# Optimization experiments

Measured on AMD Instinct MI355X. Metric: run time of the kernel, lower is better.

The kernel has to match this reference:

```python
import jax, jax.numpy as jnp
import numpy as np

N_USER = 805   # herbs
N_ITEM = 390   # symptoms
N = 1195       # total nodes
D = 64         # embedding_dim (forced by final matmul)
E = 1_000_000
E_SUB = 500_000
B = 2048
BN_EPS = 1e-5


def _gcn(x, W, b, edge):
    # GCNConv_SH: message = Linear(x_j), aggr='mean', then tanh.
    # Linear commutes with mean (bias included when in-degree>0; isolated nodes -> 0),
    # so transform nodes once, then gather->segment-mean.
    h = x @ W.T + b                      # [N, D]
    src, dst = edge[0], edge[1]
    agg = jax.ops.segment_sum(h[src], dst, num_segments=N)          # [N, D]
    cnt = jax.ops.segment_sum(jnp.ones(edge.shape[1], x.dtype), dst, num_segments=N)
    mean = agg / jnp.maximum(cnt, 1.0)[:, None]   # isolated nodes stay 0 (PyG mean aggr)
    return jnp.tanh(mean)


def _two_layer(x, W1, b1, W2, b2, edge):
    return _gcn(_gcn(x, W1, b1, edge), W2, b2, edge)


def _norm(x, axis):
    # self.Norm(emb, count, n_dim): L2 normalize along n_dim (0 for user side, 1 for item side)
    return x / jnp.linalg.norm(x, axis=axis, keepdims=True)


def setup_inputs() -> dict:
    key = jax.random.key(0)
    ks = jax.random.split(key, 12)
    emb = jax.random.normal(ks[0], (N, D), jnp.float32)
    s = 1.0 / np.sqrt(D)
    W1 = jax.random.normal(ks[1], (D, D), jnp.float32) * s
    b1 = jnp.zeros((D,), jnp.float32)
    W2 = jax.random.normal(ks[2], (D, D), jnp.float32) * s
    b2 = jnp.zeros((D,), jnp.float32)
    mlp_W = jax.random.normal(ks[3], (64, D), jnp.float32) * s
    mlp_b = jnp.zeros((64,), jnp.float32)
    bn_gamma = jnp.ones((64,), jnp.float32)
    bn_beta = jnp.zeros((64,), jnp.float32)
    # multi-hot prescription; guarantee nonzero row sums for the mean-pool divide
    presc = (jax.random.uniform(ks[4], (B, N_ITEM)) < 0.05).astype(jnp.float32)
    presc = presc.at[:, 0].set(1.0)
    total_g = jax.random.randint(ks[5], (2, E), 0, N)
    sub_g1 = jax.random.randint(ks[6], (2, E_SUB), 0, N)
    sub_g2 = jax.random.randint(ks[7], (2, E_SUB), 0, N)
    edge_index_SH = jax.random.randint(ks[8], (2, 1000), 0, N)
    return {"edge_index_SH": edge_index_SH, "prescription": presc,
            "emb": emb, "W1": W1, "b1": b1, "W2": W2, "b2": b2,
            "mlp_W": mlp_W, "mlp_b": mlp_b, "bn_gamma": bn_gamma, "bn_beta": bn_beta,
            "total_g": total_g, "sub_g1": sub_g1, "sub_g2": sub_g2}


def reference(edge_index_SH, prescription, emb, W1, b1, W2, b2, mlp_W, mlp_b,
              bn_gamma, bn_beta, total_g, sub_g1, sub_g2):
    # edge_index_SH is accepted (forward signature) but unused, as in the source.
    x_SH1 = emb                                   # SH_embedding(arange(1195))
    x_SH6 = _two_layer(emb, W1, b1, W2, b2, total_g)   # two shared GCNConv_SH layers
    SH_g3 = _two_layer(emb, W1, b1, W2, b2, sub_g1)
    SH_g33 = _two_layer(emb, W1, b1, W2, b2, sub_g2)

    # ssl_layer_loss returns normalized previous (raw-embedding) views
    s_u = _norm(x_SH1[:N_USER], 0)   # [805, D]
    s_i = _norm(x_SH1[N_USER:], 1)   # [390, D]
    # sgl_loss returns normalized sub-graph-1 views
    n_u = _norm(SH_g3[:N_USER], 0)
    n_i = _norm(SH_g3[N_USER:], 1)
    # Same2Loss (reconstructed): fuse all contrastive views into final node reps
    c_u = 0.25 * (s_i + n_i + _norm(x_SH6[N_USER:], 1) + _norm(SH_g33[N_USER:], 1))  # [390, D]
    c_i = 0.25 * (s_u + n_u + _norm(x_SH6[:N_USER], 0) + _norm(SH_g33[:N_USER], 0))  # [805, D]

    e_synd = prescription @ c_u                           # [B, D]
    e_synd = e_synd / prescription.sum(axis=1, keepdims=True)
    h = e_synd @ mlp_W.T + mlp_b                          # [B, 64]
    mu = h.mean(axis=0)
    var = h.var(axis=0)                                   # biased, as torch BN training
    h = (h - mu) / jnp.sqrt(var + BN_EPS) * bn_gamma + bn_beta
    h = jax.nn.relu(h)
    pre = h @ c_i.T                                       # [B, 805]
    return pre
```

## Files before the change

### kernel.cpp

```cpp
#include <hip/hip_runtime.h>
#include <hip/hip_bf16.h>


#define NN    1195
#define NUSER 805
#define NITEM 390
#define DD    64
#define BB    2048
#define NPAD  1216
#define E_TOT 1000000
#define E_SUB 500000
#define MT    19
#define KT    8
#define CHUNK 3
#define LSTR  72
#define OUT2STRIDE (NN*DD)
#define CPG    299
#define P8W    152
#define ROWS   96
#define RB     13
#define FNT    13
#define KPAD   448
#define ENT    7

typedef unsigned int uint;
typedef unsigned short u16;
typedef unsigned char u8;
typedef __attribute__((ext_vector_type(8))) short short8;
typedef __attribute__((ext_vector_type(4))) float f32x4;

__device__ __forceinline__ float wsum(float v) {
#pragma unroll
    for (int m = 32; m > 0; m >>= 1) v += __shfl_xor(v, m, 64);
    return v;
}
__device__ __forceinline__ u16 f2b(float f) {
    uint u = __float_as_uint(f);
    return (u16)((u + 0x7FFFu + ((u >> 16) & 1u)) >> 16);
}
__device__ __forceinline__ float b2f16(u16 b) { return __uint_as_float(((uint)b) << 16); }
__device__ __forceinline__ void split4(const float* v, u16* hh, u16* ll) {
#pragma unroll
    for (int j = 0; j < 4; ++j) {
        u16 h = f2b(v[j]);
        hh[j] = h;
        ll[j] = f2b(v[j] - b2f16(h));
    }
}
__device__ __forceinline__ uint2 pack4(const u16* x) {
    uint2 o;
    o.x = (uint)x[0] | ((uint)x[1] << 16);
    o.y = (uint)x[2] | ((uint)x[3] << 16);
    return o;
}

#define CVT_EMB   0
#define CVT_W1    76480
#define CVT_B1    80576
#define CVT_W2    80640
#define CVT_B2    84736
#define CVT_MLPW  84800
#define CVT_MLPB  88896
#define CVT_GAMMA 88960
#define CVT_BETA  89024
#define CVT_TOTAL 89088

constexpr size_t alignUp64(size_t x) { return (x + 63) & ~size_t(63); }
constexpr size_t OFF_BNS  = 0;
constexpr size_t OFF_CNSS = 128;
constexpr size_t OFF_FLAG = 384;
constexpr size_t OFF_CVT  = 448;
constexpr size_t OFF_ABF  = alignUp64(OFF_CVT + CVT_TOTAL);
constexpr size_t OFF_RC   = alignUp64(OFF_ABF + (3ull * NN * NPAD) / 2);
constexpr size_t OFF_POOL = alignUp64(OFF_RC + 3ull * NPAD);
constexpr size_t OFF_PART = OFF_POOL;
constexpr size_t OFF_H1   = alignUp64(OFF_PART + (size_t)KT * 3 * NPAD * 64);
constexpr size_t OFF_H2   = alignUp64(OFF_H1 + 64ull * NPAD);
constexpr size_t OFF_OUT2 = alignUp64(OFF_H2 + 3ull * 64 * NPAD);
constexpr size_t OFF_CU   = alignUp64(OFF_OUT2 + 3ull * NN * DD);
constexpr size_t OFF_CI   = alignUp64(OFF_CU + 448ull * DD);
constexpr size_t OFF_H    = alignUp64(OFF_CI + (size_t)NUSER * DD);
constexpr size_t POOL_END = alignUp64(OFF_H + (size_t)BB * DD);


__global__ __launch_bounds__(512) void k_front(const void* presc, const void* emb,
        const void* p1, const void* p2, const void* p3, const void* p4,
        const void* p5, const void* p6, const void* p7, const void* p8, const void* p9,
        const int* __restrict__ tg, const int* __restrict__ s1, const int* __restrict__ s2,
        float* __restrict__ dst, float* __restrict__ cnss, float* __restrict__ bnsum,
        int* __restrict__ flag, uint* __restrict__ P8, int S, int HB) {
    __shared__ __align__(16) uint lds[ROWS * P8W];
    int b = blockIdx.x, t = threadIdx.x;
    int isbf = (((const u16*)presc)[0] == 0x3F80u) ? 1 : 0;
    if (b < HB) {
        int p = b % S;
        int rg = b / S;
        int r = rg % RB;
        int g = rg / RB;
        int r0 = r * ROWS;
        {
            uint4* l4 = (uint4*)lds;
            for (int i = t; i < (ROWS * P8W) >> 2; i += 512) l4[i] = (uint4){0u, 0u, 0u, 0u};
        }
        __syncthreads();
        const int* eg = (g == 0) ? tg : (g == 1 ? s1 : s2);
        int Eg = (g == 0) ? E_TOT : E_SUB;
        int e0 = (int)(((long)p * Eg / S) & ~3L);
        int e1 = (p == S - 1) ? Eg : (int)(((long)(p + 1) * Eg / S) & ~3L);
        const int* srcp = eg;
        const int* dstp = eg + Eg;
        for (int i = e0 + t * 4; i < e1; i += 512 * 4) {
            int4 d4 = *(const int4*)(dstp + i);
            int4 s4 = *(const int4*)(srcp + i);
            int rw;
            rw = d4.x - r0; if ((unsigned)rw < ROWS) atomicAdd(&lds[rw * P8W + (s4.x >> 3)], 1u << ((s4.x & 7) * 4));
            rw = d4.y - r0; if ((unsigned)rw < ROWS) atomicAdd(&lds[rw * P8W + (s4.y >> 3)], 1u << ((s4.y & 7) * 4));
            rw = d4.z - r0; if ((unsigned)rw < ROWS) atomicAdd(&lds[rw * P8W + (s4.z >> 3)], 1u << ((s4.z & 7) * 4));
            rw = d4.w - r0; if ((unsigned)rw < ROWS) atomicAdd(&lds[rw * P8W + (s4.w >> 3)], 1u << ((s4.w & 7) * 4));
        }
        __syncthreads();
        int rmax = ROWS; if (r0 + rmax > NN) rmax = NN - r0;
        uint* out = P8 + ((size_t)p * 3 + g) * NN * P8W + (size_t)r0 * P8W;
        int n4 = (rmax * P8W) >> 2;
        const uint4* l4 = (const uint4*)lds;
        uint4* o4 = (uint4*)out;
        for (int i = t; i < n4; i += 512) o4[i] = l4[i];
    } else if (b == HB) {
        for (int i = t; i < 192; i += 512) cnss[64 + i] = 0.0f;
        if (t < 128) bnsum[t] = 0.0f;
        int c = t & 63, chunk = t >> 6;
        float s = 0.0f;
        const u16* e16 = (const u16*)emb;
        const float* e32 = (const float*)emb;
        for (int r = chunk; r < NUSER; r += 8) {
            float v = isbf ? b2f16(e16[r * 64 + c]) : e32[r * 64 + c];
            s = fmaf(v, v, s);
        }
        float* sd = (float*)lds;
        sd[t] = s;
        __syncthreads();
        if (t < 64) {
            float tot = 0.0f;
#pragma unroll
            for (int j = 0; j < 8; ++j) tot += sd[j * 64 + t];
            cnss[t] = tot;
        }
    } else {
        int i = (b - HB - 1) * 512 + t;
        if (i == 0) *flag = isbf;
        if (i < CVT_TOTAL) {
            const void* s2p; int o2;
            if      (i < CVT_W1)    { s2p = p1; o2 = i; }
            else if (i < CVT_B1)    { s2p = p2; o2 = i - CVT_W1; }
            else if (i < CVT_W2)    { s2p = p3; o2 = i - CVT_B1; }
            else if (i < CVT_B2)    { s2p = p4; o2 = i - CVT_W2; }
            else if (i < CVT_MLPW)  { s2p = p5; o2 = i - CVT_B2; }
            else if (i < CVT_MLPB)  { s2p = p6; o2 = i - CVT_MLPW; }
            else if (i < CVT_GAMMA) { s2p = p7; o2 = i - CVT_MLPB; }
            else if (i < CVT_BETA)  { s2p = p8; o2 = i - CVT_GAMMA; }
            else                    { s2p = p9; o2 = i - CVT_BETA; }
            dst[i] = isbf ? __bfloat162float(((const __hip_bfloat16*)s2p)[o2])
                          : ((const float*)s2p)[o2];
        }
    }
}

__device__ __forceinline__ void xf2_body(int g, int n0, int t,
        const float* xsrc, size_t xgstride,
        const float* part, const float* rcnt, int fromPart, int rowlim,
        const float* W, const float* bias,
        u16* Hhi, u16* Hlo, size_t hgstride, int ostride,
        u16* Ah, u16* Al, u16* Bh, u16* Bl, float* bs) {
    int w = t >> 6, l = t & 63;
    if (t < 64) bs[t] = bias ? bias[t] : 0.0f;
    int r = t >> 2, c0 = (t & 3) * 16;
    {
        const float* Wr = W + r * 64 + c0;
        float av[16];
#pragma unroll
        for (int j4 = 0; j4 < 4; ++j4) {
            float4 v = *(const float4*)(Wr + j4 * 4);
            av[j4*4+0] = v.x; av[j4*4+1] = v.y; av[j4*4+2] = v.z; av[j4*4+3] = v.w;
        }
#pragma unroll
        for (int j4 = 0; j4 < 4; ++j4) {
            u16 hh[4], ll[4];
            split4(av + j4*4, hh, ll);
            *(uint2*)(Ah + r * LSTR + c0 + j4*4) = pack4(hh);
            *(uint2*)(Al + r * LSTR + c0 + j4*4) = pack4(ll);
        }
    }
    {
        int node = n0 + r;
        float xr[16];
#pragma unroll
        for (int j = 0; j < 16; ++j) xr[j] = 0.0f;
        if (node < rowlim) {
            if (fromPart) {
#pragma unroll
                for (int k = 0; k < KT; ++k) {
                    const float* pp = part + (((size_t)k * 3 + g) * NPAD + node) * 64 + c0;
#pragma unroll
                    for (int j4 = 0; j4 < 4; ++j4) {
                        float4 v = *(const float4*)(pp + j4 * 4);
                        xr[j4*4+0] += v.x; xr[j4*4+1] += v.y;
                        xr[j4*4+2] += v.z; xr[j4*4+3] += v.w;
                    }
                }
                float rc = rcnt[g * NPAD + node];
#pragma unroll
                for (int j = 0; j < 16; ++j) xr[j] = tanhf(xr[j] * rc);
            } else {
                const float* Xr = xsrc + xgstride * g + (size_t)node * 64 + c0;
#pragma unroll
                for (int j4 = 0; j4 < 4; ++j4) {
                    float4 v = *(const float4*)(Xr + j4 * 4);
                    xr[j4*4+0] = v.x; xr[j4*4+1] = v.y;
                    xr[j4*4+2] = v.z; xr[j4*4+3] = v.w;
                }
            }
        }
#pragma unroll
        for (int j4 = 0; j4 < 4; ++j4) {
            u16 hh[4], ll[4];
            split4(xr + j4*4, hh, ll);
            *(uint2*)(Bh + r * LSTR + c0 + j4*4) = pack4(hh);
            *(uint2*)(Bl + r * LSTR + c0 + j4*4) = pack4(ll);
        }
    }
    __syncthreads();
    f32x4 acc[4];
#pragma unroll
    for (int p = 0; p < 4; ++p) acc[p] = (f32x4){0.f, 0.f, 0.f, 0.f};
    int mrow = w * 16 + (l & 15);
    int q8 = (l >> 4) * 8;
#pragma unroll
    for (int ks = 0; ks < 2; ++ks) {
        short8 ah = *(const short8*)(Ah + mrow * LSTR + ks * 32 + q8);
        short8 al = *(const short8*)(Al + mrow * LSTR + ks * 32 + q8);
#pragma unroll
        for (int p = 0; p < 4; ++p) {
            int nrow = p * 16 + (l & 15);
            short8 bh = *(const short8*)(Bh + nrow * LSTR + ks * 32 + q8);
            short8 bl = *(const short8*)(Bl + nrow * LSTR + ks * 32 + q8);
            acc[p] = __builtin_amdgcn_mfma_f32_16x16x32_bf16(ah, bh, acc[p], 0, 0, 0);
            acc[p] = __builtin_amdgcn_mfma_f32_16x16x32_bf16(ah, bl, acc[p], 0, 0, 0);
            acc[p] = __builtin_amdgcn_mfma_f32_16x16x32_bf16(al, bh, acc[p], 0, 0, 0);
        }
    }
    int q = l >> 4;
#pragma unroll
    for (int p = 0; p < 4; ++p) {
        int node = n0 + p * 16 + (l & 15);
#pragma unroll
        for (int rr2 = 0; rr2 < 4; ++rr2) {
            int d = w * 16 + q * 4 + rr2;
            float v = acc[p][rr2] + bs[d];
            u16 h = f2b(v);
            size_t o = hgstride * g + (size_t)d * ostride + node;
            Hhi[o] = h;
            Hlo[o] = f2b(v - b2f16(h));
        }
    }
}

__global__ __launch_bounds__(256) void k_xf2(const float* __restrict__ xsrc,
        size_t xgstride, const float* __restrict__ part, const float* __restrict__ rcnt,
        int fromPart, int ngb, int rowlim,
        const float* __restrict__ W, const float* __restrict__ bias,
        u16* __restrict__ Hhi, u16* __restrict__ Hlo, size_t hgstride, int ostride) {
    __shared__ u16 Ah[64 * LSTR], Al[64 * LSTR], Bh[64 * LSTR], Bl[64 * LSTR];
    __shared__ float bs[64];
    int b = blockIdx.x;
    xf2_body(b / ngb, (b % ngb) * 64, threadIdx.x, xsrc, xgstride, part, rcnt,
             fromPart, rowlim, W, bias, Hhi, Hlo, hgstride, ostride,
             Ah, Al, Bh, Bl, bs);
}

__global__ __launch_bounds__(256) void k_abf_xf1(const uint* __restrict__ P8, int S,
        u16* __restrict__ Abf, float* __restrict__ rcnt,
        const float* __restrict__ embF, const float* __restrict__ W1,
        const float* __restrict__ b1, u16* __restrict__ H1hi, u16* __restrict__ H1lo) {
    __shared__ u16 Ah[64 * LSTR], Al[64 * LSTR], Bh[64 * LSTR], Bl[64 * LSTR];
    __shared__ float bs[64];
    __shared__ float ws4[4];
    int b = blockIdx.x, t = threadIdx.x;
    if (b < 3 * NN) {
        int g = b / NN, m = b % NN;
        int w = t >> 6;
        float partial = 0.0f;
        if (t < P8W) {
            uint cnt[8] = {0, 0, 0, 0, 0, 0, 0, 0};
            for (int p = 0; p < S; ++p) {
                uint v = P8[(((size_t)p * 3 + g) * NN + m) * P8W + t];
#pragma unroll
                for (int k = 0; k < 8; ++k) cnt[k] += (v >> (4 * k)) & 15u;
            }
            uint4 o;
            o.x = (uint)f2b((float)cnt[0]) | ((uint)f2b((float)cnt[1]) << 16);
            o.y = (uint)f2b((float)cnt[2]) | ((uint)f2b((float)cnt[3]) << 16);
            o.z = (uint)f2b((float)cnt[4]) | ((uint)f2b((float)cnt[5]) << 16);
            o.w = (uint)f2b((float)cnt[6]) | ((uint)f2b((float)cnt[7]) << 16);
            *(uint4*)(Abf + (size_t)b * NPAD + t * 8) = o;
#pragma unroll
            for (int k = 0; k < 8; ++k) partial += (float)cnt[k];
        }
        partial = wsum(partial);
        if ((t & 63) == 0) ws4[w] = partial;
        __syncthreads();
        if (t == 0)
            rcnt[g * NPAD + m] = 1.0f / fmaxf(ws4[0] + ws4[1] + ws4[2] + ws4[3], 1.0f);
    } else {
        int nt = b - 3 * NN;
        xf2_body(0, nt * 64, t, embF, 0, nullptr, nullptr, 0, NN, W1, b1,
                 H1hi, H1lo, 0, NPAD, Ah, Al, Bh, Bl, bs);
    }
}

__global__ __launch_bounds__(256) void k_aggp(const u16* __restrict__ Abf,
        const u16* __restrict__ Hhi, const u16* __restrict__ Hlo, size_t hstride,
        float* __restrict__ part) {
    int b = blockIdx.x;
    int kt = b & 7;
    int mt = (b >> 3) % MT;
    int g  = (b >> 3) / MT;
    int t = threadIdx.x, w = t >> 6, l = t & 63;
    __shared__ u16 As[64 * LSTR], Bh[64 * LSTR], Bl[64 * LSTR];
    f32x4 acc[4];
#pragma unroll
    for (int p = 0; p < 4; ++p) acc[p] = (f32x4){0.f, 0.f, 0.f, 0.f};
    int m0 = mt * 64;
    const u16* Ag = Abf + (size_t)g * NN * NPAD;
    const u16* Hg = Hhi + hstride * g;
    const u16* Lg = Hlo + hstride * g;
    int st0 = kt * CHUNK;
    int st1 = st0 + CHUNK; if (st1 > MT) st1 = MT;
    int rr = t >> 4, c4 = (t & 15) * 4;
    for (int st = st0; st < st1; ++st) {
        int s0 = st * 64;
        __syncthreads();
#pragma unroll
        for (int pass = 0; pass < 4; ++pass) {
            int r = pass * 16 + rr;
            uint2 av = {0u, 0u};
            if (m0 + r < NN) av = *(const uint2*)(Ag + (size_t)(m0 + r) * NPAD + s0 + c4);
            *(uint2*)(As + r * LSTR + c4) = av;
            *(uint2*)(Bh + r * LSTR + c4) = *(const uint2*)(Hg + (size_t)r * NPAD + s0 + c4);
            *(uint2*)(Bl + r * LSTR + c4) = *(const uint2*)(Lg + (size_t)r * NPAD + s0 + c4);
        }
        __syncthreads();
        int mrow = w * 16 + (l & 15);
        int q8 = (l >> 4) * 8;
#pragma unroll
        for (int ks = 0; ks < 2; ++ks) {
            short8 a = *(const short8*)(As + mrow * LSTR + ks * 32 + q8);
#pragma unroll
            for (int p = 0; p < 4; ++p) {
                int nrow = p * 16 + (l & 15);
                short8 bh = *(const short8*)(Bh + nrow * LSTR + ks * 32 + q8);
                short8 bl = *(const short8*)(Bl + nrow * LSTR + ks * 32 + q8);
                acc[p] = __builtin_amdgcn_mfma_f32_16x16x32_bf16(a, bh, acc[p], 0, 0, 0);
                acc[p] = __builtin_amdgcn_mfma_f32_16x16x32_bf16(a, bl, acc[p], 0, 0, 0);
            }
        }
    }
    int q = l >> 4;
#pragma unroll
    for (int p = 0; p < 4; ++p) {
        int n = p * 16 + (l & 15);
#pragma unroll
        for (int r = 0; r < 4; ++r) {
            int m = m0 + w * 16 + q * 4 + r;
            if (m < NN)
                part[(((size_t)kt * 3 + g) * NPAD + m) * 64 + n] = acc[p][r];
        }
    }
}

__global__ __launch_bounds__(256) void k_comb(const float* __restrict__ part,
        const float* __restrict__ rcnt, float* __restrict__ out, float* __restrict__ cnss) {
    int g = blockIdx.x / CPG, bi = blockIdx.x % CPG;
    int t = threadIdx.x;
    int idx = bi * 256 + t;
    int m = idx >> 6, n = idx & 63;
    bool valid = idx < NN * 64;
    float v = 0.0f;
    if (valid) {
        float s = 0.0f;
#pragma unroll
        for (int k = 0; k < KT; ++k)
            s += part[(((size_t)k * 3 + g) * NPAD + m) * 64 + n];
        v = tanhf(s * rcnt[g * NPAD + m]);
        out[(size_t)g * NN * 64 + idx] = v;
    }
    float x2 = (valid && m < NUSER) ? v * v : 0.0f;
    __shared__ float sd[256];
    sd[t] = x2;
    __syncthreads();
    if (t < 64) {
        float s = sd[t] + sd[t + 64] + sd[t + 128] + sd[t + 192];
        if (s != 0.0f) atomicAdd(&cnss[(g + 1) * 64 + t], s);
    }
}

__global__ void k_cuci(const float* __restrict__ embf, const float* __restrict__ out2,
                       const float* __restrict__ cnss, float* __restrict__ cu,
                       float* __restrict__ ci) {
    int b = blockIdx.x, l = threadIdx.x;
    if (b < 448) {
        if (b >= NITEM) { cu[(size_t)b * DD + l] = 0.0f; return; }
        int node = NUSER + b;
        const float* v0 = embf + (size_t)node * DD;
        const float* v1 = out2 + (size_t)node * DD;
        const float* v2 = out2 + OUT2STRIDE + (size_t)node * DD;
        const float* v3 = out2 + 2ull * OUT2STRIDE + (size_t)node * DD;
        float total = 0.0f;
        { float x = v0[l]; float ss = wsum(x * x); total += x / sqrtf(ss); }
        { float x = v1[l]; float ss = wsum(x * x); total += x / sqrtf(ss); }
        { float x = v2[l]; float ss = wsum(x * x); total += x / sqrtf(ss); }
        { float x = v3[l]; float ss = wsum(x * x); total += x / sqrtf(ss); }
        cu[(size_t)b * DD + l] = 0.25f * total;
    } else {
        int u = b - 448;
        size_t i = (size_t)u * DD + l;
        float s = embf[i] / sqrtf(cnss[l])
                + out2[i] / sqrtf(cnss[64 + l])
                + out2[OUT2STRIDE + i] / sqrtf(cnss[128 + l])
                + out2[2ull * OUT2STRIDE + i] / sqrtf(cnss[192 + l]);
        ci[i] = 0.25f * s;
    }
}

__global__ __launch_bounds__(256) void k_esynd(const void* __restrict__ presc,
        const u16* __restrict__ cwh, const u16* __restrict__ cwl,
        const float* __restrict__ mlpB, const int* __restrict__ flag,
        float* __restrict__ hpre, float* __restrict__ bnsum) {
    int m0 = blockIdx.x * 64;
    int t = threadIdx.x, w = t >> 6, l = t & 63;
    int isbf = *flag;
    const u16* pB = (const u16*)presc;
    const float* pF = (const float*)presc;
    __shared__ u16 As[64 * LSTR], Bh[64 * LSTR], Bl[64 * LSTR];
    __shared__ u16 Ones[16 * LSTR];
    __shared__ float bs[64];
    __shared__ float r1[4][64], r2[4][64];
    for (int i = t; i < 16 * LSTR; i += 256) Ones[i] = (i < 64) ? 0x3F80u : 0u;
    if (t < 64) bs[t] = mlpB[t];

    f32x4 acc[4], acc1;
#pragma unroll
    for (int p = 0; p < 4; ++p) acc[p] = (f32x4){0.f, 0.f, 0.f, 0.f};
    acc1 = (f32x4){0.f, 0.f, 0.f, 0.f};

    int rr = t >> 4, c4 = (t & 15) * 4;
    for (int st = 0; st < ENT; ++st) {
        int s0 = st * 64;
        __syncthreads();
#pragma unroll
        for (int pass = 0; pass < 4; ++pass) {
            int r = pass * 16 + rr;
            int m = m0 + r;
            int kb = s0 + c4;
            u16 a4[4];
            if (kb + 3 < NITEM) {
                if (isbf) {
                    const uint* p32 = (const uint*)pB + (((size_t)m * NITEM + kb) >> 1);
                    uint u0 = p32[0], u1 = p32[1];
                    a4[0] = (u16)u0; a4[1] = (u16)(u0 >> 16);
                    a4[2] = (u16)u1; a4[3] = (u16)(u1 >> 16);
                } else {
                    const float2* pf2 = (const float2*)(pF + (size_t)m * NITEM + kb);
                    float2 f0 = pf2[0], f1 = pf2[1];
                    a4[0] = f2b(f0.x); a4[1] = f2b(f0.y);
                    a4[2] = f2b(f1.x); a4[3] = f2b(f1.y);
                }
            } else {
#pragma unroll
                for (int j = 0; j < 4; ++j) {
                    int k = kb + j;
                    a4[j] = (k < NITEM)
                          ? (isbf ? pB[(size_t)m * NITEM + k] : f2b(pF[(size_t)m * NITEM + k]))
                          : (u16)0;
                }
            }
            uint2 o;
            o.x = (uint)a4[0] | ((uint)a4[1] << 16);
            o.y = (uint)a4[2] | ((uint)a4[3] << 16);
            *(uint2*)(As + r * LSTR + c4) = o;
            *(uint2*)(Bh + r * LSTR + c4) = *(const uint2*)(cwh + (size_t)r * KPAD + s0 + c4);
            *(uint2*)(Bl + r * LSTR + c4) = *(const uint2*)(cwl + (size_t)r * KPAD + s0 + c4);
        }
        __syncthreads();
        int mrow = w * 16 + (l & 15);
        int q8 = (l >> 4) * 8;
#pragma unroll
        for (int ks = 0; ks < 2; ++ks) {
            short8 a = *(const short8*)(As + mrow * LSTR + ks * 32 + q8);
            short8 on = *(const short8*)(Ones + (l & 15) * LSTR + ks * 32 + q8);
            acc1 = __builtin_amdgcn_mfma_f32_16x16x32_bf16(a, on, acc1, 0, 0, 0);
#pragma unroll
            for (int p = 0; p < 4; ++p) {
                int nrow = p * 16 + (l & 15);
                short8 bh = *(const short8*)(Bh + nrow * LSTR + ks * 32 + q8);
                short8 bl = *(const short8*)(Bl + nrow * LSTR + ks * 32 + q8);
                acc[p] = __builtin_amdgcn_mfma_f32_16x16x32_bf16(a, bh, acc[p], 0, 0, 0);
                acc[p] = __builtin_amdgcn_mfma_f32_16x16x32_bf16(a, bl, acc[p], 0, 0, 0);
            }
        }
    }
    float inv[4];
#pragma unroll
    for (int r = 0; r < 4; ++r)
        inv[r] = 1.0f / __shfl(acc1[r], l & 48, 64);
    int q = l >> 4;
#pragma unroll
    for (int p = 0; p < 4; ++p) {
        int col = p * 16 + (l & 15);
        float a = 0.0f, c = 0.0f;
#pragma unroll
        for (int r = 0; r < 4; ++r) {
            float hv = acc[p][r] * inv[r] + bs[col];
            hpre[(size_t)(m0 + w * 16 + q * 4 + r) * DD + col] = hv;
            a += hv; c = fmaf(hv, hv, c);
        }
        a += __shfl_xor(a, 16, 64); a += __shfl_xor(a, 32, 64);
        c += __shfl_xor(c, 16, 64); c += __shfl_xor(c, 32, 64);
        if (l < 16) { r1[w][col] = a; r2[w][col] = c; }
    }
    __syncthreads();
    if (t < 64) {
        atomicAdd(&bnsum[t],      r1[0][t] + r1[1][t] + r1[2][t] + r1[3][t]);
        atomicAdd(&bnsum[64 + t], r2[0][t] + r2[1][t] + r2[2][t] + r2[3][t]);
    }
}

__global__ __launch_bounds__(256) void k_final(const float* __restrict__ hpre,
        const float* __restrict__ bnsum, const float* __restrict__ gamma,
        const float* __restrict__ beta, const float* __restrict__ ci,
        void* __restrict__ out, const int* __restrict__ flag) {
    int b = blockIdx.x;
    int mt = b / FNT, nt = b % FNT;
    int m0 = mt * 64, n0 = nt * 64;
    int t = threadIdx.x, w = t >> 6, l = t & 63;
    __shared__ u16 Ah[64 * LSTR], Al[64 * LSTR], Bh[64 * LSTR], Bl[64 * LSTR];
    __shared__ float mn[64], rsg[64], bt[64];
    if (t < 64) {
        float mean = bnsum[t] * (1.0f / BB);
        float var = bnsum[64 + t] * (1.0f / BB) - mean * mean;
        mn[t] = mean;
        rsg[t] = gamma[t] / sqrtf(var + 1e-5f);
        bt[t] = beta[t];
    }
    __syncthreads();
    const float4* hp4 = (const float4*)(hpre + (size_t)m0 * 64);
    const float4* ci4 = (const float4*)ci;
#pragma unroll
    for (int k = 0; k < 4; ++k) {
        int i = t + k * 256;
        int r = i >> 4, c4 = (i & 15) * 4;
        float4 v = hp4[i];
        float vv[4] = {v.x, v.y, v.z, v.w};
        u16 hh[4], ll[4];
#pragma unroll
        for (int j = 0; j < 4; ++j) {
            int d = c4 + j;
            float x = fmaxf((vv[j] - mn[d]) * rsg[d] + bt[d], 0.0f);
            u16 hb = f2b(x);
            hh[j] = hb;
            ll[j] = f2b(x - b2f16(hb));
        }
        *(uint2*)(Ah + r * LSTR + c4) = pack4(hh);
        *(uint2*)(Al + r * LSTR + c4) = pack4(ll);
        int col = n0 + r;
        float4 cv = (col < NUSER) ? ci4[(size_t)col * 16 + (i & 15)]
                                  : (float4){0.f, 0.f, 0.f, 0.f};
        float cc[4] = {cv.x, cv.y, cv.z, cv.w};
        split4(cc, hh, ll);
        *(uint2*)(Bh + r * LSTR + c4) = pack4(hh);
        *(uint2*)(Bl + r * LSTR + c4) = pack4(ll);
    }
    __syncthreads();
    f32x4 acc[4];
#pragma unroll
    for (int p = 0; p < 4; ++p) acc[p] = (f32x4){0.f, 0.f, 0.f, 0.f};
    int mrow = w * 16 + (l & 15);
    int q8 = (l >> 4) * 8;
#pragma unroll
    for (int ks = 0; ks < 2; ++ks) {
        short8 ah = *(const short8*)(Ah + mrow * LSTR + ks * 32 + q8);
        short8 al = *(const short8*)(Al + mrow * LSTR + ks * 32 + q8);
#pragma unroll
        for (int p = 0; p < 4; ++p) {
            int nrow = p * 16 + (l & 15);
            short8 bh = *(const short8*)(Bh + nrow * LSTR + ks * 32 + q8);
            short8 bl = *(const short8*)(Bl + nrow * LSTR + ks * 32 + q8);
            acc[p] = __builtin_amdgcn_mfma_f32_16x16x32_bf16(ah, bh, acc[p], 0, 0, 0);
            acc[p] = __builtin_amdgcn_mfma_f32_16x16x32_bf16(ah, bl, acc[p], 0, 0, 0);
            acc[p] = __builtin_amdgcn_mfma_f32_16x16x32_bf16(al, bh, acc[p], 0, 0, 0);
        }
    }
    int isbf = *flag;
    int q = l >> 4;
#pragma unroll
    for (int p = 0; p < 4; ++p) {
        int col = n0 + p * 16 + (l & 15);
        if (col < NUSER) {
#pragma unroll
            for (int r = 0; r < 4; ++r) {
                int row = m0 + w * 16 + q * 4 + r;
                size_t o = (size_t)row * NUSER + col;
                if (isbf) ((__hip_bfloat16*)out)[o] = __float2bfloat16(acc[p][r]);
                else      ((float*)out)[o] = acc[p][r];
            }
        }
    }
}

extern "C" void kernel_launch(void* const* d_in, const int* in_sizes, int n_in,
                              void* d_out, int out_size, void* d_ws, size_t ws_size,
                              hipStream_t stream) {
    const void* presc = d_in[1];
    const void* emb   = d_in[2];
    const void* W1    = d_in[3];
    const void* b1    = d_in[4];
    const void* W2    = d_in[5];
    const void* b2    = d_in[6];
    const void* mlpW  = d_in[7];
    const void* mlpB  = d_in[8];
    const void* gamma = d_in[9];
    const void* beta  = d_in[10];
    const int* tg = (const int*)d_in[11];
    const int* s1 = (const int*)d_in[12];
    const int* s2 = (const int*)d_in[13];
    float* ws = (float*)d_ws;
    (void)in_sizes; (void)n_in; (void)out_size;

    float* bnsum = ws + OFF_BNS;
    float* cnss  = ws + OFF_CNSS;
    int*   flag  = (int*)(ws + OFF_FLAG);
    float* cvt   = ws + OFF_CVT;
    float* embF  = cvt + CVT_EMB;
    float* W1F   = cvt + CVT_W1;
    float* b1F   = cvt + CVT_B1;
    float* W2F   = cvt + CVT_W2;
    float* b2F   = cvt + CVT_B2;
    float* mlpWF = cvt + CVT_MLPW;
    float* mlpBF = cvt + CVT_MLPB;
    float* gamF  = cvt + CVT_GAMMA;
    float* betF  = cvt + CVT_BETA;
    u16*   Abf   = (u16*)(ws + OFF_ABF);
    float* rcnt  = ws + OFF_RC;
    uint*  P8    = (uint*)(ws + OFF_POOL);
    float* part  = ws + OFF_PART;
    u16*   H1hi  = (u16*)(ws + OFF_H1);
    u16*   H1lo  = H1hi + 64ull * NPAD;
    u16*   H2hi  = (u16*)(ws + OFF_H2);
    u16*   H2lo  = H2hi + 3ull * 64 * NPAD;
    float* out2  = ws + OFF_OUT2;
    float* cu    = ws + OFF_CU;
    float* ci    = ws + OFF_CI;
    float* hpre  = ws + OFF_H;
    u16*   cwh   = (u16*)(ws + OFF_PART);
    u16*   cwl   = cwh + 64ull * KPAD;

    size_t p8per = 3ull * NN * P8W;
    int S = 4;
    if      (ws_size >= (OFF_POOL + 16ull * p8per) * 4) S = 16;
    else if (ws_size >= (OFF_POOL +  8ull * p8per) * 4) S = 8;
    int HB = 3 * RB * S;
    int CVTB = CVT_TOTAL / 512;

    k_front<<<HB + 1 + CVTB, 512, 0, stream>>>(presc, emb,
        emb, W1, b1, W2, b2, mlpW, mlpB, gamma, beta,
        tg, s1, s2, cvt, cnss, bnsum, flag, P8, S, HB);
    k_abf_xf1<<<3 * NN + MT, 256, 0, stream>>>(P8, S, Abf, rcnt,
        embF, W1F, b1F, H1hi, H1lo);
    k_aggp<<<3 * MT * KT, 256, 0, stream>>>(Abf, H1hi, H1lo, 0, part);
    k_xf2<<<3 * MT, 256, 0, stream>>>(nullptr, 0, part, rcnt, 1, MT, NN,
        W2F, b2F, H2hi, H2lo, 64ull * NPAD, NPAD);
    k_aggp<<<3 * MT * KT, 256, 0, stream>>>(Abf, H2hi, H2lo, 64ull * NPAD, part);
    k_comb<<<3 * CPG, 256, 0, stream>>>(part, rcnt, out2, cnss);
    k_cuci<<<448 + NUSER, 64, 0, stream>>>(embF, out2, cnss, cu, ci);
    k_xf2<<<ENT, 256, 0, stream>>>(cu, 0, nullptr, nullptr, 0, ENT, 448,
        mlpWF, nullptr, cwh, cwl, 0, KPAD);
    k_esynd<<<BB / 64, 256, 0, stream>>>(presc, cwh, cwl, mlpBF, flag, hpre, bnsum);
    k_final<<<(BB / 64) * FNT, 256, 0, stream>>>(hpre, bnsum, gamF, betF, ci, d_out, flag);
}
```

Baseline: 229.6 us.

## Rebalance edge histogram blocks: per-graph split counts, larger row tiles, 1024 threads

The front histogram kernel now splits the edge list into different numbers of partitions per graph: the total graph gets twice as many as each subgraph, so the per-block edge work is balanced. Blocks grow to 1024 threads and use dynamic LDS so each block can cover 128 destination rows where the attribute allows, which cuts the number of row passes over the edge list. The workspace layout is computed at run time from the copy count, and the reduction kernel indexes copies by a per-graph base. The trade-off is fewer, larger blocks with more LDS each, which may lower occupancy, and the larger copy count depends on workspace size.

```diff
diff --git a/kernel.cpp b/kernel.cpp
--- a/kernel.cpp
+++ b/kernel.cpp
@@ -17,8 +17,6 @@
 #define OUT2STRIDE (NN*DD)
 #define CPG    299
 #define P8W    152
-#define ROWS   96
-#define RB     13
 #define FNT    13
 #define KPAD   448
 #define ENT    7
@@ -73,66 +71,63 @@
 constexpr size_t OFF_ABF  = alignUp64(OFF_CVT + CVT_TOTAL);
 constexpr size_t OFF_RC   = alignUp64(OFF_ABF + (3ull * NN * NPAD) / 2);
 constexpr size_t OFF_POOL = alignUp64(OFF_RC + 3ull * NPAD);
-constexpr size_t OFF_PART = OFF_POOL;
-constexpr size_t OFF_H1   = alignUp64(OFF_PART + (size_t)KT * 3 * NPAD * 64);
-constexpr size_t OFF_H2   = alignUp64(OFF_H1 + 64ull * NPAD);
-constexpr size_t OFF_OUT2 = alignUp64(OFF_H2 + 3ull * 64 * NPAD);
-constexpr size_t OFF_CU   = alignUp64(OFF_OUT2 + 3ull * NN * DD);
-constexpr size_t OFF_CI   = alignUp64(OFF_CU + 448ull * DD);
-constexpr size_t OFF_H    = alignUp64(OFF_CI + (size_t)NUSER * DD);
-constexpr size_t POOL_END = alignUp64(OFF_H + (size_t)BB * DD);
-
-
-__global__ __launch_bounds__(512) void k_front(const void* presc, const void* emb,
+
+
+__global__ __launch_bounds__(1024, 8) void k_front(const void* presc, const void* emb,
         const void* p1, const void* p2, const void* p3, const void* p4,
         const void* p5, const void* p6, const void* p7, const void* p8, const void* p9,
         const int* __restrict__ tg, const int* __restrict__ s1, const int* __restrict__ s2,
         float* __restrict__ dst, float* __restrict__ cnss, float* __restrict__ bnsum,
-        int* __restrict__ flag, uint* __restrict__ P8, int S, int HB) {
-    __shared__ __align__(16) uint lds[ROWS * P8W];
+        int* __restrict__ flag, uint* __restrict__ P8,
+        int S0, int S1, int R, int rows, int HB) {
+    extern __shared__ __align__(16) uint lds[];
     int b = blockIdx.x, t = threadIdx.x;
     int isbf = (((const u16*)presc)[0] == 0x3F80u) ? 1 : 0;
     if (b < HB) {
-        int p = b % S;
-        int rg = b / S;
-        int r = rg % RB;
-        int g = rg / RB;
-        int r0 = r * ROWS;
+        int RS0 = R * S0, RS1 = R * S1;
+        int g, p, r;
+        if (b < RS0)            { g = 0; p = b % S0; r = b / S0; }
+        else if (b < RS0 + RS1) { int b2 = b - RS0;        g = 1; p = b2 % S1; r = b2 / S1; }
+        else                    { int b3 = b - RS0 - RS1;  g = 2; p = b3 % S1; r = b3 / S1; }
+        int Sg = g ? S1 : S0;
+        int cb = (g == 0) ? 0 : S0 + (g - 1) * S1;
+        int r0 = r * rows;
+        int nw4 = (rows * P8W) >> 2;
         {
             uint4* l4 = (uint4*)lds;
-            for (int i = t; i < (ROWS * P8W) >> 2; i += 512) l4[i] = (uint4){0u, 0u, 0u, 0u};
+            for (int i = t; i < nw4; i += 1024) l4[i] = (uint4){0u, 0u, 0u, 0u};
         }
         __syncthreads();
         const int* eg = (g == 0) ? tg : (g == 1 ? s1 : s2);
         int Eg = (g == 0) ? E_TOT : E_SUB;
-        int e0 = (int)(((long)p * Eg / S) & ~3L);
-        int e1 = (p == S - 1) ? Eg : (int)(((long)(p + 1) * Eg / S) & ~3L);
+        int e0 = (int)(((long)p * Eg / Sg) & ~3L);
+        int e1 = (p == Sg - 1) ? Eg : (int)(((long)(p + 1) * Eg / Sg) & ~3L);
         const int* srcp = eg;
         const int* dstp = eg + Eg;
-        for (int i = e0 + t * 4; i < e1; i += 512 * 4) {
+        for (int i = e0 + t * 4; i < e1; i += 1024 * 4) {
             int4 d4 = *(const int4*)(dstp + i);
             int4 s4 = *(const int4*)(srcp + i);
             int rw;
-            rw = d4.x - r0; if ((unsigned)rw < ROWS) atomicAdd(&lds[rw * P8W + (s4.x >> 3)], 1u << ((s4.x & 7) * 4));
-            rw = d4.y - r0; if ((unsigned)rw < ROWS) atomicAdd(&lds[rw * P8W + (s4.y >> 3)], 1u << ((s4.y & 7) * 4));
-            rw = d4.z - r0; if ((unsigned)rw < ROWS) atomicAdd(&lds[rw * P8W + (s4.z >> 3)], 1u << ((s4.z & 7) * 4));
-            rw = d4.w - r0; if ((unsigned)rw < ROWS) atomicAdd(&lds[rw * P8W + (s4.w >> 3)], 1u << ((s4.w & 7) * 4));
+            rw = d4.x - r0; if ((unsigned)rw < (unsigned)rows) atomicAdd(&lds[rw * P8W + (s4.x >> 3)], 1u << ((s4.x & 7) * 4));
+            rw = d4.y - r0; if ((unsigned)rw < (unsigned)rows) atomicAdd(&lds[rw * P8W + (s4.y >> 3)], 1u << ((s4.y & 7) * 4));
+            rw = d4.z - r0; if ((unsigned)rw < (unsigned)rows) atomicAdd(&lds[rw * P8W + (s4.z >> 3)], 1u << ((s4.z & 7) * 4));
+            rw = d4.w - r0; if ((unsigned)rw < (unsigned)rows) atomicAdd(&lds[rw * P8W + (s4.w >> 3)], 1u << ((s4.w & 7) * 4));
         }
         __syncthreads();
-        int rmax = ROWS; if (r0 + rmax > NN) rmax = NN - r0;
-        uint* out = P8 + ((size_t)p * 3 + g) * NN * P8W + (size_t)r0 * P8W;
+        int rmax = rows; if (r0 + rmax > NN) rmax = NN - r0;
+        uint* out = P8 + ((size_t)(cb + p) * NN + r0) * P8W;
         int n4 = (rmax * P8W) >> 2;
         const uint4* l4 = (const uint4*)lds;
         uint4* o4 = (uint4*)out;
-        for (int i = t; i < n4; i += 512) o4[i] = l4[i];
+        for (int i = t; i < n4; i += 1024) o4[i] = l4[i];
     } else if (b == HB) {
-        for (int i = t; i < 192; i += 512) cnss[64 + i] = 0.0f;
+        if (t < 192) cnss[64 + t] = 0.0f;
         if (t < 128) bnsum[t] = 0.0f;
         int c = t & 63, chunk = t >> 6;
         float s = 0.0f;
         const u16* e16 = (const u16*)emb;
         const float* e32 = (const float*)emb;
-        for (int r = chunk; r < NUSER; r += 8) {
+        for (int r = chunk; r < NUSER; r += 16) {
             float v = isbf ? b2f16(e16[r * 64 + c]) : e32[r * 64 + c];
             s = fmaf(v, v, s);
         }
@@ -142,11 +137,11 @@
         if (t < 64) {
             float tot = 0.0f;
 #pragma unroll
-            for (int j = 0; j < 8; ++j) tot += sd[j * 64 + t];
+            for (int j = 0; j < 16; ++j) tot += sd[j * 64 + t];
             cnss[t] = tot;
         }
     } else {
-        int i = (b - HB - 1) * 512 + t;
+        int i = (b - HB - 1) * 1024 + t;
         if (i == 0) *flag = isbf;
         if (i < CVT_TOTAL) {
             const void* s2p; int o2;
@@ -277,7 +272,8 @@
              Ah, Al, Bh, Bl, bs);
 }
 
-__global__ __launch_bounds__(256) void k_abf_xf1(const uint* __restrict__ P8, int S,
+__global__ __launch_bounds__(256) void k_abf_xf1(const uint* __restrict__ P8,
+        int S0, int S1,
         u16* __restrict__ Abf, float* __restrict__ rcnt,
         const float* __restrict__ embF, const float* __restrict__ W1,
         const float* __restrict__ b1, u16* __restrict__ H1hi, u16* __restrict__ H1lo) {
@@ -287,12 +283,14 @@
     int b = blockIdx.x, t = threadIdx.x;
     if (b < 3 * NN) {
         int g = b / NN, m = b % NN;
+        int Sg = g ? S1 : S0;
+        int cb = (g == 0) ? 0 : S0 + (g - 1) * S1;
         int w = t >> 6;
         float partial = 0.0f;
         if (t < P8W) {
             uint cnt[8] = {0, 0, 0, 0, 0, 0, 0, 0};
-            for (int p = 0; p < S; ++p) {
-                uint v = P8[(((size_t)p * 3 + g) * NN + m) * P8W + t];
+            for (int p = 0; p < Sg; ++p) {
+                uint v = P8[((size_t)(cb + p) * NN + m) * P8W + t];
 #pragma unroll
                 for (int k = 0; k < 8; ++k) cnt[k] += (v >> (4 * k)) & 15u;
             }
@@ -651,29 +649,44 @@
     u16*   Abf   = (u16*)(ws + OFF_ABF);
     float* rcnt  = ws + OFF_RC;
     uint*  P8    = (uint*)(ws + OFF_POOL);
-    float* part  = ws + OFF_PART;
-    u16*   H1hi  = (u16*)(ws + OFF_H1);
-    u16*   H1lo  = H1hi + 64ull * NPAD;
-    u16*   H2hi  = (u16*)(ws + OFF_H2);
-    u16*   H2lo  = H2hi + 3ull * 64 * NPAD;
-    float* out2  = ws + OFF_OUT2;
-    float* cu    = ws + OFF_CU;
-    float* ci    = ws + OFF_CI;
-    float* hpre  = ws + OFF_H;
-    u16*   cwh   = (u16*)(ws + OFF_PART);
+    float* part  = ws + OFF_POOL;
+    u16*   cwh   = (u16*)(ws + OFF_POOL);
     u16*   cwl   = cwh + 64ull * KPAD;
 
-    size_t p8per = 3ull * NN * P8W;
-    int S = 4;
-    if      (ws_size >= (OFF_POOL + 16ull * p8per) * 4) S = 16;
-    else if (ws_size >= (OFF_POOL +  8ull * p8per) * 4) S = 8;
-    int HB = 3 * RB * S;
-    int CVTB = CVT_TOTAL / 512;
-
-    k_front<<<HB + 1 + CVTB, 512, 0, stream>>>(presc, emb,
+    static int g_rows = 0;
+    if (g_rows == 0) {
+        hipError_t e = hipFuncSetAttribute((const void*)k_front,
+                hipFuncAttributeMaxDynamicSharedMemorySize, 128 * P8W * 4);
+        g_rows = (e == hipSuccess) ? 128 : 96;
+    }
+    int rows = g_rows;
+    int R = (NN + rows - 1) / rows;
+
+    size_t cpw = (size_t)NN * P8W;
+    size_t tailF = 760000;
+    int SU = 1;
+    if      ((OFF_POOL + 32 * cpw + tailF) * 4 <= ws_size) SU = 4;
+    else if ((OFF_POOL + 16 * cpw + tailF) * 4 <= ws_size) SU = 2;
+    int S0 = 4 * SU, S1 = 2 * SU;
+    int copies = S0 + 2 * S1;
+
+    size_t o = alignUp64(OFF_POOL + (size_t)copies * cpw);
+    u16*   H1hi = (u16*)(ws + o);  u16* H1lo = H1hi + 64ull * NPAD;
+    o = alignUp64(o + 64ull * NPAD);
+    u16*   H2hi = (u16*)(ws + o);  u16* H2lo = H2hi + 3ull * 64 * NPAD;
+    o = alignUp64(o + 3ull * 64 * NPAD);
+    float* out2 = ws + o;          o = alignUp64(o + 3ull * NN * DD);
+    float* cu   = ws + o;          o = alignUp64(o + 448ull * DD);
+    float* ci   = ws + o;          o = alignUp64(o + (size_t)NUSER * DD);
+    float* hpre = ws + o;
+
+    int HB = R * copies;
+    int CVTB = CVT_TOTAL / 1024;
+
+    k_front<<<HB + 1 + CVTB, 1024, rows * P8W * 4, stream>>>(presc, emb,
         emb, W1, b1, W2, b2, mlpW, mlpB, gamma, beta,
-        tg, s1, s2, cvt, cnss, bnsum, flag, P8, S, HB);
-    k_abf_xf1<<<3 * NN + MT, 256, 0, stream>>>(P8, S, Abf, rcnt,
+        tg, s1, s2, cvt, cnss, bnsum, flag, P8, S0, S1, R, rows, HB);
+    k_abf_xf1<<<3 * NN + MT, 256, 0, stream>>>(P8, S0, S1, Abf, rcnt,
         embF, W1F, b1F, H1hi, H1lo);
     k_aggp<<<3 * MT * KT, 256, 0, stream>>>(Abf, H1hi, H1lo, 0, part);
     k_xf2<<<3 * MT, 256, 0, stream>>>(nullptr, 0, part, rcnt, 1, MT, NN,
```

Measured after the change: 197.7 us. 13.9% less time.
